# Kernel tuning notes

Hardware: AMD Instinct MI355X
Metric: run time of the kernel (lower is better)

Reference implementation:

```python
import jax, jax.numpy as jnp
import numpy as np
import math

C = 512          # channels
K = 3            # conv kernel size
DILATIONS = (1, 3, 5)
RATIO = 2        # up/down sample ratio
FK = 12          # FIR anti-alias kernel size


def kaiser_sinc_filter1d(cutoff, half_width, kernel_size):
    # BigVGAN alias-free kaiser-windowed sinc lowpass filter
    half_size = kernel_size // 2
    delta_f = 4.0 * half_width
    A = 2.285 * (half_size - 1) * math.pi * delta_f + 7.95
    if A > 50.0:
        beta = 0.1102 * (A - 8.7)
    elif A >= 21.0:
        beta = 0.5842 * (A - 21.0) ** 0.4 + 0.07886 * (A - 21.0)
    else:
        beta = 0.0
    window = np.kaiser(kernel_size, beta)
    if kernel_size % 2 == 0:
        time = np.arange(-half_size, half_size) + 0.5
    else:
        time = np.arange(kernel_size) - half_size
    filt = 2.0 * cutoff * window * np.sinc(2.0 * cutoff * time)
    filt = filt / filt.sum()
    return jnp.asarray(filt, dtype=jnp.float32)

# Up/Down both use cutoff=0.5/ratio, half_width=0.6/ratio, kernel=12
AA_FILTER = kaiser_sinc_filter1d(0.5 / RATIO, 0.6 / RATIO, FK)

UP_PAD = FK // RATIO - 1                               # 5 (replicate pad before transpose conv)
UP_PAD_LEFT = UP_PAD * RATIO + (FK - RATIO) // 2       # 15
UP_PAD_RIGHT = UP_PAD * RATIO + (FK - RATIO + 1) // 2  # 15
DN_PAD_LEFT = FK // 2 - 1                              # 5 (even kernel)
DN_PAD_RIGHT = FK // 2                                 # 6


def _depthwise_conv(x, filt, stride=1, lhs_dilation=1, padding=(0, 0)):
    c = x.shape[1]
    w = jnp.broadcast_to(filt.reshape(1, 1, -1), (c, 1, filt.shape[0]))
    return jax.lax.conv_general_dilated(
        x, w, window_strides=(stride,), padding=[padding],
        lhs_dilation=(lhs_dilation,), dimension_numbers=('NCH', 'OIH', 'NCH'),
        feature_group_count=c)


def upsample2x(x):
    # replicate pad, depthwise transposed conv (lhs-dilated conv w/ flipped kernel), crop, scale
    x = jnp.pad(x, ((0, 0), (0, 0), (UP_PAD, UP_PAD)), mode='edge')
    y = RATIO * _depthwise_conv(x, AA_FILTER[::-1], lhs_dilation=RATIO,
                                padding=(FK - 1, FK - 1))
    return y[..., UP_PAD_LEFT:-UP_PAD_RIGHT]


def downsample2x(x):
    x = jnp.pad(x, ((0, 0), (0, 0), (DN_PAD_LEFT, DN_PAD_RIGHT)), mode='edge')
    return _depthwise_conv(x, AA_FILTER, stride=RATIO)


def snake_log(x, alpha, beta):
    # use_log_scale=True: alpha/beta are exponentiated; x + 1/(b+1e-5) * sin(a*x)^2
    a = jnp.exp(alpha)[None, :, None]
    b = jnp.exp(beta)[None, :, None]
    return x + (1.0 / (b + 1e-5)) * jnp.square(jnp.sin(x * a))


def aliasing_activation(x, alpha, beta):
    return downsample2x(snake_log(upsample2x(x), alpha, beta))


def weight_norm_conv1d(x, v, g, bias, dilation):
    # torch weight_norm dim=0: W[o] = g[o] * v[o] / ||v[o]||
    norm = jnp.sqrt(jnp.sum(v * v, axis=(1, 2), keepdims=True))
    w = g[:, None, None] * v / norm
    pad = (K * dilation - dilation) // 2
    y = jax.lax.conv_general_dilated(
        x, w, window_strides=(1,), padding=[(pad, pad)],
        rhs_dilation=(dilation,), dimension_numbers=('NCH', 'OIH', 'NCH'))
    return y + bias[None, :, None]


def setup_inputs() -> dict:
    key = jax.random.key(0)
    ks = jax.random.split(key, 12)
    B, T = 16, 4096
    return {
        'x': jax.random.normal(ks[0], (B, C, T), dtype=jnp.float32),
        'float_masks': jnp.ones((B, 1, T), dtype=jnp.float32),
        'in_snake_alpha': 0.1 * jax.random.normal(ks[1], (3, C), dtype=jnp.float32),
        'in_snake_beta': 0.1 * jax.random.normal(ks[2], (3, C), dtype=jnp.float32),
        'out_snake_alpha': 0.1 * jax.random.normal(ks[3], (3, C), dtype=jnp.float32),
        'out_snake_beta': 0.1 * jax.random.normal(ks[4], (3, C), dtype=jnp.float32),
        'in_conv_v': 0.05 * jax.random.normal(ks[5], (3, C, C, K), dtype=jnp.float32),
        'in_conv_g': 1.0 + 0.01 * jax.random.normal(ks[6], (3, C), dtype=jnp.float32),
        'in_conv_b': 0.01 * jax.random.normal(ks[7], (3, C), dtype=jnp.float32),
        'out_conv_v': 0.05 * jax.random.normal(ks[8], (3, C, C, K), dtype=jnp.float32),
        'out_conv_g': 1.0 + 0.01 * jax.random.normal(ks[9], (3, C), dtype=jnp.float32),
        'out_conv_b': 0.01 * jax.random.normal(ks[10], (3, C), dtype=jnp.float32),
    }


def reference(x, float_masks, in_snake_alpha, in_snake_beta, out_snake_alpha,
              out_snake_beta, in_conv_v, in_conv_g, in_conv_b, out_conv_v,
              out_conv_g, out_conv_b):
    for i, dilation in enumerate(DILATIONS):
        residuals = x
        x = aliasing_activation(x, in_snake_alpha[i], in_snake_beta[i]) * float_masks
        x = weight_norm_conv1d(x, in_conv_v[i], in_conv_g[i], in_conv_b[i], dilation)
        x = aliasing_activation(x, out_snake_alpha[i], out_snake_beta[i]) * float_masks
        x = weight_norm_conv1d(x, out_conv_v[i], out_conv_g[i], out_conv_b[i], 1)
        x = x + residuals
    return x * float_masks
```

## Files before the change

kernel.cpp:

```cpp
#include <hip/hip_runtime.h>
#include <cmath>

#define BN_ 16
#define CN_ 512
#define TN_ 4096
#define TPAD_ 4112
#define PADR_ 8

typedef float f32x4 __attribute__((ext_vector_type(4)));
typedef __bf16 bf16x8 __attribute__((ext_vector_type(8)));
typedef unsigned short u16x8 __attribute__((ext_vector_type(8)));

struct AAFilt { float g0[6]; float g1[6]; float fE[6]; float fO[6]; };

__device__ __forceinline__ unsigned short f2bf(float f) {
  unsigned u = __builtin_bit_cast(unsigned, f);
  u = (u + 0x7fffu + ((u >> 16) & 1u)) >> 16;
  return (unsigned short)u;
}
__device__ __forceinline__ float bf2f(unsigned short h) {
  return __builtin_bit_cast(float, (unsigned)h << 16);
}
__device__ __forceinline__ float to_f(float x) { return x; }
__device__ __forceinline__ float to_f(unsigned short x) { return bf2f(x); }

__device__ __forceinline__ void gld16(const void* g, void* l) {
  __builtin_amdgcn_global_load_lds((const __attribute__((address_space(1))) void*)g,
                                   (__attribute__((address_space(3))) void*)l,
                                   16, 0, 0);
}

__global__ __launch_bounds__(256) void prep_w(
    const float* __restrict__ vin, const float* __restrict__ gin,
    const float* __restrict__ vout, const float* __restrict__ gout,
    unsigned short* __restrict__ wpack)
{
  const int o = blockIdx.x;
  const int l = blockIdx.y;
  const int i = l >> 1, oc = l & 1;
  const float* v = (oc ? vout : vin) + (size_t)i * CN_ * CN_ * 3 + (size_t)o * CN_ * 3;
  const float g = (oc ? gout : gin)[i * CN_ + o];
  const int tid = threadIdx.x;

  float a = 0.f;
  for (int j = tid; j < 1536; j += 256) { float x = v[j]; a += x * x; }
  #pragma unroll
  for (int off = 32; off > 0; off >>= 1) a += __shfl_down(a, off);
  __shared__ float red[4];
  if ((tid & 63) == 0) red[tid >> 6] = a;
  __syncthreads();
  const float tot = red[0] + red[1] + red[2] + red[3];
  const float scale = g / sqrtf(tot);
  unsigned short* wl = wpack + (size_t)l * 3 * CN_ * CN_;
  for (int j = tid; j < 1536; j += 256) {
    int c = j / 3, k = j - 3 * c;
    wl[((size_t)k * CN_ + o) * CN_ + c] = f2bf(v[j] * scale);
  }
}

__global__ __launch_bounds__(256) void transpose_in(
    const float* __restrict__ src, float* __restrict__ dst)
{
  __shared__ float tile[32][33];
  const int b = blockIdx.z, c0 = blockIdx.y * 32, t0 = blockIdx.x * 32;
  const int tx = threadIdx.x & 31, ty = threadIdx.x >> 5;
  const float* s = src + ((size_t)b * CN_ + c0) * TN_ + t0;
  #pragma unroll
  for (int j = 0; j < 32; j += 8) tile[ty + j][tx] = s[(size_t)(ty + j) * TN_ + tx];
  __syncthreads();
  float* d = dst + ((size_t)b * TN_ + t0) * CN_ + c0;
  #pragma unroll
  for (int j = 0; j < 32; j += 8) d[(size_t)(ty + j) * CN_ + tx] = tile[tx][ty + j];
}

template <typename TIN>
__global__ __launch_bounds__(512) void act_kernel(
    const TIN* __restrict__ src, unsigned short* __restrict__ dst,
    const float* __restrict__ alpha, const float* __restrict__ beta,
    const float* __restrict__ mask, AAFilt F)
{
  const int c = threadIdx.x;
  const int b = blockIdx.y;
  const int seg = blockIdx.x;
  const int t0 = seg << 7;
  const float av = expf(alpha[c]);
  const float ib = 1.0f / (expf(beta[c]) + 1e-5f);
  const TIN* row = src + (size_t)b * TN_ * CN_ + c;
  unsigned short* drow = dst + (size_t)b * TPAD_ * CN_ + c;
  const float* mrow = mask + (size_t)b * TN_;

  if (seg == 0)  { for (int p = 0; p < PADR_; ++p) drow[(size_t)p * CN_] = 0; }
  if (seg == 31) { for (int p = 0; p < PADR_; ++p) drow[(size_t)(TPAD_ - PADR_ + p) * CN_] = 0; }

  auto ldx = [&](int t) -> float {
    t = t < 0 ? 0 : (t > TN_ - 1 ? TN_ - 1 : t);
    return to_f(row[(size_t)t * CN_]);
  };

  float xw[6];
  #pragma unroll
  for (int j = 0; j < 6; ++j) xw[j] = ldx(t0 - 5 + j);
  float sE[6], sO[6];
  #pragma unroll
  for (int j = 0; j < 6; ++j) { sE[j] = 0.f; sO[j] = 0.f; }
  float s_last = 0.f;

  auto step = [&](int tau, bool emit) {
    float uO = 0.f, uE = 0.f;
    #pragma unroll
    for (int j = 0; j < 6; ++j) { uO += F.g1[j] * xw[j]; uE += F.g0[j] * xw[j]; }
    float so = __sinf(uO * av); float sOn = uO + ib * so * so;
    float se = __sinf(uE * av); float sEn = uE + ib * se * se;
    if (tau + 2 == TN_ - 1) s_last = sOn;
    if (tau + 2 >= TN_) sOn = s_last;
    if (tau + 3 >= TN_) sEn = s_last;
    #pragma unroll
    for (int j = 0; j < 5; ++j) { sE[j] = sE[j + 1]; sO[j] = sO[j + 1]; }
    sE[5] = sEn; sO[5] = sOn;
    if (emit) {
      float d = 0.f;
      #pragma unroll
      for (int j = 0; j < 6; ++j) d += F.fE[j] * sE[j] + F.fO[j] * sO[j];
      d *= mrow[tau];
      drow[(size_t)(PADR_ + tau) * CN_] = f2bf(d);
    }
    #pragma unroll
    for (int j = 0; j < 5; ++j) xw[j] = xw[j + 1];
    xw[5] = ldx(tau + 6);
  };

  for (int w = 0; w < 5; ++w) step(t0 - 5 + w, false);
  if (t0 == 0) {
    float s0 = sE[3];
    sE[1] = s0; sE[2] = s0;
    sO[1] = s0; sO[2] = s0; sO[3] = s0;
  }
  for (int t = t0; t < t0 + 128; ++t) step(t, true);
}

template <int MODE>
__global__ __launch_bounds__(256) void conv_kernel(
    const unsigned short* __restrict__ act,
    const unsigned short* __restrict__ wp,
    const float* __restrict__ bias,
    const float* __restrict__ res,
    const float* __restrict__ mask,
    void* __restrict__ outp, int dil)
{
  __shared__ __align__(16) unsigned short lA[144 * 32];
  __shared__ __align__(16) unsigned short lB[3 * 128 * 32];
  const int tid = threadIdx.x;
  const int b = blockIdx.x >> 5;
  const int t0 = (blockIdx.x & 31) << 7;
  const int o0 = blockIdx.y << 7;
  const int lane = tid & 63;
  const int wave = tid >> 6;
  const int wm = wave >> 1, wn = wave & 1;

  const f32x4 zero = {0.f, 0.f, 0.f, 0.f};
  f32x4 acc[4][4];
  #pragma unroll
  for (int a = 0; a < 4; ++a)
    #pragma unroll
    for (int n = 0; n < 4; ++n) acc[a][n] = zero;

  const unsigned short* aBase = act + ((size_t)b * TPAD_ + t0) * CN_;

  for (int cb = 0; cb < 16; ++cb) {
    const int c0 = cb * 32;
    #pragma unroll
    for (int it = 0; it < 3; ++it) {
      int p = tid + it * 256;
      if (p < 576) {
        int r = p >> 2, pq = p & 3;
        int gq = pq ^ (r & 3);
        gld16(aBase + (size_t)r * CN_ + c0 + gq * 8, lA + (size_t)p * 8);
      }
    }
    #pragma unroll
    for (int it = 0; it < 6; ++it) {
      int p = tid + it * 256;
      int k = p >> 9, rem = p & 511, ol = rem >> 2, pq = rem & 3;
      int gq = pq ^ (ol & 3);
      gld16(wp + ((size_t)k * CN_ + o0 + ol) * CN_ + c0 + gq * 8, lB + (size_t)p * 8);
    }
    __syncthreads();

    #pragma unroll
    for (int k = 0; k < 3; ++k) {
      const int rb = wm * 64 + (lane & 15) + PADR_ + (k - 1) * dil;
      bf16x8 af[4], bfr[4];
      #pragma unroll
      for (int mi = 0; mi < 4; ++mi) {
        int r = rb + mi * 16;
        int q = (lane >> 4) ^ (r & 3);
        af[mi] = __builtin_bit_cast(bf16x8, *reinterpret_cast<const u16x8*>(lA + ((size_t)r * 4 + q) * 8));
      }
      #pragma unroll
      for (int ni = 0; ni < 4; ++ni) {
        int ol = wn * 64 + ni * 16 + (lane & 15);
        int q = (lane >> 4) ^ (ol & 3);
        bfr[ni] = __builtin_bit_cast(bf16x8, *reinterpret_cast<const u16x8*>(lB + (((size_t)k * 128 + ol) * 4 + q) * 8));
      }
      #pragma unroll
      for (int mi = 0; mi < 4; ++mi)
        #pragma unroll
        for (int ni = 0; ni < 4; ++ni)
          acc[mi][ni] = __builtin_amdgcn_mfma_f32_16x16x32_bf16(af[mi], bfr[ni], acc[mi][ni], 0, 0, 0);
    }
    __syncthreads();
  }

  const int olane = lane & 15, rg = lane >> 4;
  const int obase = o0 + wn * 64 + olane;
  const int tbase = t0 + wm * 64 + rg * 4;

  if (MODE == 0) {
    unsigned short* O = (unsigned short*)outp + (size_t)b * TN_ * CN_;
    #pragma unroll
    for (int ni = 0; ni < 4; ++ni) {
      float bv = bias[obase + ni * 16];
      #pragma unroll
      for (int mi = 0; mi < 4; ++mi) {
        #pragma unroll
        for (int r = 0; r < 4; ++r) {
          int t = tbase + mi * 16 + r;
          O[(size_t)t * CN_ + obase + ni * 16] = f2bf(acc[mi][ni][r] + bv);
        }
      }
    }
  } else if (MODE == 1) {
    float* O = (float*)outp + (size_t)b * TN_ * CN_;
    const float* R = res + (size_t)b * TN_ * CN_;
    #pragma unroll
    for (int ni = 0; ni < 4; ++ni) {
      float bv = bias[obase + ni * 16];
      #pragma unroll
      for (int mi = 0; mi < 4; ++mi) {
        #pragma unroll
        for (int r = 0; r < 4; ++r) {
          int t = tbase + mi * 16 + r;
          size_t ix = (size_t)t * CN_ + obase + ni * 16;
          O[ix] = acc[mi][ni][r] + bv + R[ix];
        }
      }
    }
  } else {
    float* O = (float*)outp + (size_t)b * CN_ * TN_;
    const float* R = res + (size_t)b * TN_ * CN_;
    const float* M = mask + (size_t)b * TN_;
    float bv[4];
    #pragma unroll
    for (int ni = 0; ni < 4; ++ni) bv[ni] = bias[obase + ni * 16];
    #pragma unroll
    for (int mi = 0; mi < 4; ++mi) {
      int t = tbase + mi * 16;
      f32x4 mv = *reinterpret_cast<const f32x4*>(M + t);
      #pragma unroll
      for (int ni = 0; ni < 4; ++ni) {
        f32x4 v;
        #pragma unroll
        for (int r = 0; r < 4; ++r)
          v[r] = (acc[mi][ni][r] + bv[ni] + R[(size_t)(t + r) * CN_ + obase + ni * 16]) * mv[r];
        *reinterpret_cast<f32x4*>(O + (size_t)(obase + ni * 16) * TN_ + t) = v;
      }
    }
  }
}

static double bi0(double x) {
  double s = 1.0, t = 1.0, q = x * x * 0.25;
  for (int k = 1; k < 50; ++k) { t *= q / ((double)k * (double)k); s += t; if (t < 1e-18 * s) break; }
  return s;
}
static void make_filt(AAFilt* F) {
  const double PI = 3.14159265358979323846;
  double A = 2.285 * 5.0 * PI * 1.2 + 7.95;
  double beta;
  if (A > 50.0) beta = 0.1102 * (A - 8.7);
  else if (A >= 21.0) beta = 0.5842 * pow(A - 21.0, 0.4) + 0.07886 * (A - 21.0);
  else beta = 0.0;
  double i0b = bi0(beta);
  double f[12], sum = 0.0;
  for (int n = 0; n < 12; ++n) {
    double xx = 2.0 * n / 11.0 - 1.0;
    double w = bi0(beta * sqrt(fmax(0.0, 1.0 - xx * xx))) / i0b;
    double tt = (double)(n - 6) + 0.5;
    double arg = 0.5 * tt;
    double snc = sin(PI * arg) / (PI * arg);
    f[n] = 0.5 * w * snc;
    sum += f[n];
  }
  for (int n = 0; n < 12; ++n) f[n] /= sum;
  for (int j = 0; j < 6; ++j) {
    F->g0[j] = (float)(2.0 * f[11 - 2 * j]);
    F->g1[j] = (float)(2.0 * f[10 - 2 * j]);
    F->fE[j] = (float)f[2 * j + 1];
    F->fO[j] = (float)f[2 * j];
  }
}

extern "C" void kernel_launch(void* const* d_in, const int* in_sizes, int n_in,
                              void* d_out, int out_size, void* d_ws, size_t ws_size,
                              hipStream_t stream)
{
  (void)in_sizes; (void)n_in; (void)out_size; (void)ws_size;
  const float* x    = (const float*)d_in[0];
  const float* mask = (const float*)d_in[1];
  const float* inA  = (const float*)d_in[2];
  const float* inB  = (const float*)d_in[3];
  const float* outA = (const float*)d_in[4];
  const float* outB = (const float*)d_in[5];
  const float* vin  = (const float*)d_in[6];
  const float* gin  = (const float*)d_in[7];
  const float* bin  = (const float*)d_in[8];
  const float* vout = (const float*)d_in[9];
  const float* gout = (const float*)d_in[10];
  const float* bout = (const float*)d_in[11];

  char* ws = (char*)d_ws;
  float* xta          = (float*)ws;
  unsigned short* actb = (unsigned short*)(ws + 134217728);
  unsigned short* y1   = (unsigned short*)(ws + 134217728 + 67371008);
  unsigned short* wpk  = (unsigned short*)(ws + 134217728 + 67371008 + 67108864);

  AAFilt F; make_filt(&F);

  prep_w<<<dim3(512, 6), dim3(256), 0, stream>>>(vin, gin, vout, gout, wpk);
  transpose_in<<<dim3(128, 16, 16), dim3(256), 0, stream>>>(x, xta);

  const int dils[3] = {1, 3, 5};
  float* xcur = xta;
  float* dof = (float*)d_out;
  for (int i = 0; i < 3; ++i) {
    act_kernel<float><<<dim3(32, 16), dim3(512), 0, stream>>>(
        xcur, actb, inA + i * CN_, inB + i * CN_, mask, F);
    conv_kernel<0><<<dim3(512, 4), dim3(256), 0, stream>>>(
        actb, wpk + (size_t)(2 * i) * 3 * CN_ * CN_, bin + i * CN_,
        nullptr, mask, (void*)y1, dils[i]);
    act_kernel<unsigned short><<<dim3(32, 16), dim3(512), 0, stream>>>(
        y1, actb, outA + i * CN_, outB + i * CN_, mask, F);
    if (i < 2) {
      float* xnext = (i == 0) ? dof : xta;
      conv_kernel<1><<<dim3(512, 4), dim3(256), 0, stream>>>(
          actb, wpk + (size_t)(2 * i + 1) * 3 * CN_ * CN_, bout + i * CN_,
          xcur, mask, (void*)xnext, 1);
      xcur = xnext;
    } else {
      conv_kernel<2><<<dim3(512, 4), dim3(256), 0, stream>>>(
          actb, wpk + (size_t)(2 * i + 1) * 3 * CN_ * CN_, bout + i * CN_,
          xcur, mask, d_out, 1);
    }
  }
}
```

Measured before the change: 1.292 ms.

## Enlarge conv tiles to 256x256, double-buffer LDS, add XCD-aware block mapping

```diff
diff --git a/kernel.cpp b/kernel.cpp
--- a/kernel.cpp
+++ b/kernel.cpp
@@ -138,8 +138,11 @@
   for (int t = t0; t < t0 + 128; ++t) step(t, true);
 }
 
+#define ASZ (272 * 32)
+#define BSZ (3 * 256 * 32)
+
 template <int MODE>
-__global__ __launch_bounds__(256) void conv_kernel(
+__global__ __launch_bounds__(512, 2) void conv_kernel(
     const unsigned short* __restrict__ act,
     const unsigned short* __restrict__ wp,
     const float* __restrict__ bias,
@@ -147,73 +150,93 @@
     const float* __restrict__ mask,
     void* __restrict__ outp, int dil)
 {
-  __shared__ __align__(16) unsigned short lA[144 * 32];
-  __shared__ __align__(16) unsigned short lB[3 * 128 * 32];
+  __shared__ __align__(16) unsigned short lA[2 * ASZ];
+  __shared__ __align__(16) unsigned short lB[2 * BSZ];
+
   const int tid = threadIdx.x;
-  const int b = blockIdx.x >> 5;
-  const int t0 = (blockIdx.x & 31) << 7;
-  const int o0 = blockIdx.y << 7;
+  const int bid = blockIdx.x;
+  const int xcd = bid & 7, j = bid >> 3;
+  const int ob = j & 1, tile = j >> 1;
+  const int tt = tile * 8 + xcd;
+  const int b = tt >> 4;
+  const int t0 = (tt & 15) << 8;
+  const int o0 = ob << 8;
+
   const int lane = tid & 63;
   const int wave = tid >> 6;
-  const int wm = wave >> 1, wn = wave & 1;
+  const int wm = wave >> 2, wn = wave & 3;
 
   const f32x4 zero = {0.f, 0.f, 0.f, 0.f};
-  f32x4 acc[4][4];
-  #pragma unroll
-  for (int a = 0; a < 4; ++a)
+  f32x4 acc[8][4];
+  #pragma unroll
+  for (int a = 0; a < 8; ++a)
     #pragma unroll
     for (int n = 0; n < 4; ++n) acc[a][n] = zero;
 
   const unsigned short* aBase = act + ((size_t)b * TPAD_ + t0) * CN_;
 
+  auto stage = [&](int bufi, int cb) {
+    const int c0 = cb * 32;
+    unsigned short* A = lA + (size_t)bufi * ASZ;
+    unsigned short* B = lB + (size_t)bufi * BSZ;
+    #pragma unroll
+    for (int it = 0; it < 2; ++it) {
+      int p = tid + it * 512;
+      int r = p >> 2, pq = p & 3, gq = pq ^ (r & 3);
+      gld16(aBase + (size_t)r * CN_ + c0 + gq * 8, A + (size_t)p * 8);
+    }
+    if (tid < 64) {
+      int p = tid + 1024;
+      int r = p >> 2, pq = p & 3, gq = pq ^ (r & 3);
+      gld16(aBase + (size_t)r * CN_ + c0 + gq * 8, A + (size_t)p * 8);
+    }
+    #pragma unroll
+    for (int it = 0; it < 6; ++it) {
+      int p = tid + it * 512;
+      int k = p >> 10, rem = p & 1023, ol = rem >> 2, pq = rem & 3;
+      int gq = pq ^ (ol & 3);
+      gld16(wp + ((size_t)(k * CN_ + o0 + ol)) * CN_ + c0 + gq * 8, B + (size_t)p * 8);
+    }
+  };
+
+  stage(0, 0);
+  __syncthreads();
+
   for (int cb = 0; cb < 16; ++cb) {
-    const int c0 = cb * 32;
-    #pragma unroll
-    for (int it = 0; it < 3; ++it) {
-      int p = tid + it * 256;
-      if (p < 576) {
-        int r = p >> 2, pq = p & 3;
-        int gq = pq ^ (r & 3);
-        gld16(aBase + (size_t)r * CN_ + c0 + gq * 8, lA + (size_t)p * 8);
-      }
-    }
-    #pragma unroll
-    for (int it = 0; it < 6; ++it) {
-      int p = tid + it * 256;
-      int k = p >> 9, rem = p & 511, ol = rem >> 2, pq = rem & 3;
-      int gq = pq ^ (ol & 3);
-      gld16(wp + ((size_t)k * CN_ + o0 + ol) * CN_ + c0 + gq * 8, lB + (size_t)p * 8);
-    }
-    __syncthreads();
+    const int cur = cb & 1;
+    if (cb < 15) stage(cur ^ 1, cb + 1);
+    const unsigned short* A = lA + (size_t)cur * ASZ;
+    const unsigned short* B = lB + (size_t)cur * BSZ;
 
     #pragma unroll
     for (int k = 0; k < 3; ++k) {
-      const int rb = wm * 64 + (lane & 15) + PADR_ + (k - 1) * dil;
-      bf16x8 af[4], bfr[4];
-      #pragma unroll
-      for (int mi = 0; mi < 4; ++mi) {
-        int r = rb + mi * 16;
+      bf16x8 af[8], bfr[4];
+      #pragma unroll
+      for (int mi = 0; mi < 8; ++mi) {
+        int r = wm * 128 + (lane & 15) + mi * 16 + PADR_ + (k - 1) * dil;
         int q = (lane >> 4) ^ (r & 3);
-        af[mi] = __builtin_bit_cast(bf16x8, *reinterpret_cast<const u16x8*>(lA + ((size_t)r * 4 + q) * 8));
+        af[mi] = __builtin_bit_cast(bf16x8, *reinterpret_cast<const u16x8*>(A + ((size_t)r * 4 + q) * 8));
       }
       #pragma unroll
       for (int ni = 0; ni < 4; ++ni) {
         int ol = wn * 64 + ni * 16 + (lane & 15);
         int q = (lane >> 4) ^ (ol & 3);
-        bfr[ni] = __builtin_bit_cast(bf16x8, *reinterpret_cast<const u16x8*>(lB + (((size_t)k * 128 + ol) * 4 + q) * 8));
-      }
-      #pragma unroll
-      for (int mi = 0; mi < 4; ++mi)
+        bfr[ni] = __builtin_bit_cast(bf16x8, *reinterpret_cast<const u16x8*>(B + (((size_t)k * 256 + ol) * 4 + q) * 8));
+      }
+      __builtin_amdgcn_s_setprio(1);
+      #pragma unroll
+      for (int mi = 0; mi < 8; ++mi)
         #pragma unroll
         for (int ni = 0; ni < 4; ++ni)
           acc[mi][ni] = __builtin_amdgcn_mfma_f32_16x16x32_bf16(af[mi], bfr[ni], acc[mi][ni], 0, 0, 0);
+      __builtin_amdgcn_s_setprio(0);
     }
     __syncthreads();
   }
 
   const int olane = lane & 15, rg = lane >> 4;
   const int obase = o0 + wn * 64 + olane;
-  const int tbase = t0 + wm * 64 + rg * 4;
+  const int tbase = t0 + wm * 128 + rg * 4;
 
   if (MODE == 0) {
     unsigned short* O = (unsigned short*)outp + (size_t)b * TN_ * CN_;
@@ -221,7 +244,7 @@
     for (int ni = 0; ni < 4; ++ni) {
       float bv = bias[obase + ni * 16];
       #pragma unroll
-      for (int mi = 0; mi < 4; ++mi) {
+      for (int mi = 0; mi < 8; ++mi) {
         #pragma unroll
         for (int r = 0; r < 4; ++r) {
           int t = tbase + mi * 16 + r;
@@ -236,7 +259,7 @@
     for (int ni = 0; ni < 4; ++ni) {
       float bv = bias[obase + ni * 16];
       #pragma unroll
-      for (int mi = 0; mi < 4; ++mi) {
+      for (int mi = 0; mi < 8; ++mi) {
         #pragma unroll
         for (int r = 0; r < 4; ++r) {
           int t = tbase + mi * 16 + r;
@@ -253,7 +276,7 @@
     #pragma unroll
     for (int ni = 0; ni < 4; ++ni) bv[ni] = bias[obase + ni * 16];
     #pragma unroll
-    for (int mi = 0; mi < 4; ++mi) {
+    for (int mi = 0; mi < 8; ++mi) {
       int t = tbase + mi * 16;
       f32x4 mv = *reinterpret_cast<const f32x4*>(M + t);
       #pragma unroll
@@ -319,7 +342,7 @@
   const float* bout = (const float*)d_in[11];
 
   char* ws = (char*)d_ws;
-  float* xta          = (float*)ws;
+  float* xta           = (float*)ws;
   unsigned short* actb = (unsigned short*)(ws + 134217728);
   unsigned short* y1   = (unsigned short*)(ws + 134217728 + 67371008);
   unsigned short* wpk  = (unsigned short*)(ws + 134217728 + 67371008 + 67108864);
@@ -335,19 +358,19 @@
   for (int i = 0; i < 3; ++i) {
     act_kernel<float><<<dim3(32, 16), dim3(512), 0, stream>>>(
         xcur, actb, inA + i * CN_, inB + i * CN_, mask, F);
-    conv_kernel<0><<<dim3(512, 4), dim3(256), 0, stream>>>(
+    conv_kernel<0><<<dim3(512), dim3(512), 0, stream>>>(
         actb, wpk + (size_t)(2 * i) * 3 * CN_ * CN_, bin + i * CN_,
         nullptr, mask, (void*)y1, dils[i]);
     act_kernel<unsigned short><<<dim3(32, 16), dim3(512), 0, stream>>>(
         y1, actb, outA + i * CN_, outB + i * CN_, mask, F);
     if (i < 2) {
       float* xnext = (i == 0) ? dof : xta;
-      conv_kernel<1><<<dim3(512, 4), dim3(256), 0, stream>>>(
+      conv_kernel<1><<<dim3(512), dim3(512), 0, stream>>>(
           actb, wpk + (size_t)(2 * i + 1) * 3 * CN_ * CN_, bout + i * CN_,
           xcur, mask, (void*)xnext, 1);
       xcur = xnext;
     } else {
-      conv_kernel<2><<<dim3(512, 4), dim3(256), 0, stream>>>(
+      conv_kernel<2><<<dim3(512), dim3(512), 0, stream>>>(
           actb, wpk + (size_t)(2 * i + 1) * 3 * CN_ * CN_, bout + i * CN_,
           xcur, mask, d_out, 1);
     }
```

Result: faster. 1.253 ms (-3.0%).
